# Kernel optimization log

Hardware: AMD Instinct MI355X
Metric: run time of the kernel (lower is better)

Reference implementation:

```python
import jax, jax.numpy as jnp
import numpy as np

N = 8192        # nodes
E = 262144      # edges (avg degree 32)
IN_CH = 256
CH = 128
SLOPE = 0.2     # PyG GATv2Conv default negative_slope


def gatv2(x, src, dst, wl, wr, att, b):
    """Single-head GATv2Conv (PyG defaults: share_weights=False, self-loops
    already appended to src/dst). x: [N, in]; wl, wr: [out, in]; att: [out]."""
    xl = x @ wl.T                      # [N, out] source-side transform (x_j)
    xr = x @ wr.T                      # [N, out] target-side transform (x_i)
    # per-edge attention logit: att . LeakyReLU(x_l[src] + x_r[dst])
    e = jax.nn.leaky_relu(xl[src] + xr[dst], SLOPE) @ att   # [E']
    # segment softmax over incoming edges of each target node
    m = jax.ops.segment_max(e, dst, num_segments=N)
    p = jnp.exp(e - m[dst])
    s = jax.ops.segment_sum(p, dst, num_segments=N)
    alpha = p / s[dst]                 # every node has a self-loop -> s > 0
    out = jax.ops.segment_sum(alpha[:, None] * xl[src], dst, num_segments=N)
    return out + b


def setup_inputs() -> dict:
    key = jax.random.key(0)
    ks = jax.random.split(key, 2 + 5 * 3)
    inp = {
        "x": jax.random.normal(ks[0], (N, IN_CH), dtype=jnp.float32),
        "edge_index": jax.random.randint(ks[1], (2, E), 0, N, dtype=jnp.int64),
    }
    dims = [(CH, IN_CH), (2 * CH, CH), (CH, 2 * CH), (CH, 2 * CH), (IN_CH, CH)]
    ki = 2
    for i, (oc, ic) in enumerate(dims, start=1):
        sc = (2.0 / (ic + oc)) ** 0.5  # glorot-ish
        inp[f"w{i}l"] = jax.random.normal(ks[ki], (oc, ic), dtype=jnp.float32) * sc
        inp[f"w{i}r"] = jax.random.normal(ks[ki + 1], (oc, ic), dtype=jnp.float32) * sc
        inp[f"a{i}"] = jax.random.normal(ks[ki + 2], (oc,), dtype=jnp.float32) * sc
        inp[f"b{i}"] = jnp.zeros((oc,), dtype=jnp.float32)
        ki += 3
    return inp


def reference(x, edge_index,
              w1l, w1r, a1, b1,
              w2l, w2r, a2, b2,
              w3l, w3r, a3, b3,
              w4l, w4r, a4, b4,
              w5l, w5r, a5, b5):
    loops = jnp.arange(N, dtype=edge_index.dtype)
    src = jnp.concatenate([edge_index[0], loops])   # add_self_loops=True
    dst = jnp.concatenate([edge_index[1], loops])
    h = jax.nn.relu(gatv2(x, src, dst, w1l, w1r, a1, b1))          # [N, CH]
    z = jax.nn.relu(gatv2(h, src, dst, w2l, w2r, a2, b2))          # [N, 2CH]
    re = jax.nn.relu(gatv2(z, src, dst, w3l, w3r, a3, b3))         # [N, CH]
    recon_edge = jax.nn.sigmoid(re @ re.T)                         # [N, N]
    xd = jax.nn.relu(gatv2(z, src, dst, w4l, w4r, a4, b4))         # [N, CH]
    x_rec = jax.nn.relu(gatv2(xd, src, dst, w5l, w5r, a5, b5))     # [N, IN_CH]
    return recon_edge, x_rec, z
```

## Files before the change

### kernel.cpp

```cpp
#include <hip/hip_runtime.h>
#include <hip/hip_bf16.h>
#include <math.h>

#define N_NODES 8192
#define N_EDGES 262144
#define EP (N_EDGES + N_NODES)
#define SLOPE 0.2f

typedef short bf16x8 __attribute__((ext_vector_type(8)));
typedef short short4v __attribute__((ext_vector_type(4)));
typedef float f32x4 __attribute__((ext_vector_type(4)));

__global__ void extract_hist(const int* __restrict__ raw,
                             int* __restrict__ esrc, int* __restrict__ edst,
                             int* __restrict__ counts) {
    __shared__ int sflag;
    int t = threadIdx.x;
    if (t < 64) {
        unsigned long long b = __ballot(raw[2 * t + 1] != 0);
        if (t == 0) sflag = (b == 0ULL) ? 1 : 0;
    }
    __syncthreads();
    int i64f = sflag;
    int k = blockIdx.x * blockDim.x + t;
    if (k >= N_EDGES) return;
    int s, d;
    if (i64f) {
        s = raw[2 * (size_t)k];
        d = raw[2 * ((size_t)N_EDGES + k)];
    } else {
        s = raw[k];
        d = raw[N_EDGES + k];
    }
    esrc[k] = s;
    edst[k] = d;
    atomicAdd(&counts[d], 1);
}

__global__ void scan_k(const int* __restrict__ counts, int* __restrict__ row_ptr) {
    __shared__ int part[256];
    int t = threadIdx.x;
    int base = t * 32;
    int loc[32];
    int s = 0;
    for (int i = 0; i < 32; ++i) { loc[i] = s; s += counts[base + i] + 1; }
    part[t] = s;
    __syncthreads();
    for (int off = 1; off < 256; off <<= 1) {
        int tmp = (t >= off) ? part[t - off] : 0;
        __syncthreads();
        part[t] += tmp;
        __syncthreads();
    }
    int incl = part[t];
    int excl = incl - s;
    for (int i = 0; i < 32; ++i) row_ptr[base + i] = excl + loc[i];
    if (t == 255) row_ptr[N_NODES] = incl;
}

__global__ void scatter_k(const int* __restrict__ esrc, const int* __restrict__ edst,
                          const int* __restrict__ row_ptr, int* __restrict__ cursor,
                          int* __restrict__ ssrc) {
    int k = blockIdx.x * blockDim.x + threadIdx.x;
    if (k >= EP) return;
    int s, d;
    if (k < N_EDGES) { s = esrc[k]; d = edst[k]; }
    else             { s = d = k - N_EDGES; }
    int pos = row_ptr[d] + atomicAdd(&cursor[d], 1);
    ssrc[pos] = s;
}

struct WPrep {
    const float* wl[5];
    const float* wr[5];
    int oc[5];
    int lk[5];
};

__global__ void prep_all(WPrep P, const float* __restrict__ x,
                         short* __restrict__ W3all, short* __restrict__ A3) {
    int gid = blockIdx.x * blockDim.x + threadIdx.x;
    if (gid < 524288) {
        int r = gid >> 6;
        int c4 = (gid & 63) << 2;
        f32x4 a = *(const f32x4*)&x[((size_t)r << 8) + c4];
        short4v h4, l4;
#pragma unroll
        for (int j = 0; j < 4; ++j) {
            __hip_bfloat16 hb = __float2bfloat16(a[j]);
            float hf = __bfloat162float(hb);
            __hip_bfloat16 lb = __float2bfloat16(a[j] - hf);
            h4[j] = *(short*)&hb;
            l4[j] = *(short*)&lb;
        }
        size_t ro = (size_t)r * 768;
        *(short4v*)&A3[ro + c4] = h4;
        *(short4v*)&A3[ro + 256 + c4] = l4;
        *(short4v*)&A3[ro + 512 + c4] = h4;
    } else {
        int g = gid - 524288;
        int l = g >> 16;
        if (l >= 5) return;
        int rem = g & 65535;
        int lk = P.lk[l], K = 1 << lk;
        int r = rem >> lk, c = rem & (K - 1);
        int OC = P.oc[l];
        const float* w = (r < OC) ? P.wl[l] : P.wr[l];
        int rr = (r < OC) ? r : r - OC;
        float a = w[((size_t)rr << lk) + c];
        __hip_bfloat16 hb = __float2bfloat16(a);
        float hf = __bfloat162float(hb);
        __hip_bfloat16 lb = __float2bfloat16(a - hf);
        size_t ro = (size_t)l * 196608 + (size_t)r * 3 * K;
        W3all[ro + c] = *(short*)&hb;
        W3all[ro + K + c] = *(short*)&hb;
        W3all[ro + 2 * K + c] = *(short*)&lb;
    }
}

#if __has_builtin(__builtin_amdgcn_global_load_lds)
#define GL16(gsrc, lbase, lofs)                                                       \
    __builtin_amdgcn_global_load_lds((const __attribute__((address_space(1))) void*)(gsrc), \
                                     (__attribute__((address_space(3))) void*)(lbase), 16, 0, 0)
#else
#define GL16(gsrc, lbase, lofs) (*(bf16x8*)((lbase) + (lofs)) = *(const bf16x8*)(gsrc))
#endif

__global__ __launch_bounds__(256) void gemm_bf16_nt(const short* __restrict__ A3,
                                                    const short* __restrict__ W3,
                                                    float* __restrict__ C,
                                                    int K3, int N2) {
    __shared__ __align__(16) short As[2][4096];
    __shared__ __align__(16) short Bs[2][4096];
    int tid = threadIdx.x;
    int gx = gridDim.x;
    int lgx = (gx == 8) ? 3 : 2;
    int orig = blockIdx.x + (blockIdx.y << lgx);
    int nwg = gx << 7;
    int swzb = (orig & 7) * (nwg >> 3) + (orig >> 3);
    int bx = swzb & (gx - 1), by = swzb >> lgx;
    int i0 = by * 64, j0 = bx * 64;

    int wave = tid >> 6, lane = tid & 63;
    int b0 = wave * 1024 + lane * 16;
    int row0 = b0 >> 7;
    int rb0 = b0 & 127;
    int scb = rb0 ^ ((row0 & 7) << 4);
    const short* gA0 = A3 + (size_t)(i0 + row0) * K3 + (scb >> 1);
    const short* gA1 = A3 + (size_t)(i0 + row0 + 32) * K3 + (scb >> 1);
    const short* gB0 = W3 + (size_t)(j0 + row0) * K3 + (scb >> 1);
    const short* gB1 = W3 + (size_t)(j0 + row0 + 32) * K3 + (scb >> 1);
    int lofs = lane * 8;

#define STAGE(pb, k0s)                                      \
    do {                                                    \
        GL16(gA0 + (k0s), &As[pb][wave * 512], lofs);       \
        GL16(gA1 + (k0s), &As[pb][2048 + wave * 512], lofs);\
        GL16(gB0 + (k0s), &Bs[pb][wave * 512], lofs);       \
        GL16(gB1 + (k0s), &Bs[pb][2048 + wave * 512], lofs);\
    } while (0)

    int wr = (wave >> 1) * 32, wc = (wave & 1) * 32;
    int lm = lane & 15, quad = lane >> 4;
    f32x4 acc[2][2] = {};
    int nt = K3 >> 6;
    STAGE(0, 0);
    int cur = 0;
    for (int t = 0; t < nt; ++t) {
        if (t + 1 < nt) {
            STAGE(cur ^ 1, (t + 1) << 6);
            asm volatile("s_waitcnt vmcnt(4)" ::: "memory");
        } else {
            asm volatile("s_waitcnt vmcnt(0)" ::: "memory");
        }
        __builtin_amdgcn_s_barrier();
        __builtin_amdgcn_sched_barrier(0);
        const char* Ab = (const char*)&As[cur][0];
        const char* Bb = (const char*)&Bs[cur][0];
#pragma unroll
        for (int ks = 0; ks < 2; ++ks) {
            int kb = ks * 64 + quad * 16;
            bf16x8 a[2], b[2];
#pragma unroll
            for (int u = 0; u < 2; ++u) {
                int r = wr + u * 16 + lm;
                a[u] = *(const bf16x8*)(Ab + (((r << 7) | kb) ^ ((r & 7) << 4)));
            }
#pragma unroll
            for (int v = 0; v < 2; ++v) {
                int r = wc + v * 16 + lm;
                b[v] = *(const bf16x8*)(Bb + (((r << 7) | kb) ^ ((r & 7) << 4)));
            }
#pragma unroll
            for (int u = 0; u < 2; ++u)
#pragma unroll
                for (int v = 0; v < 2; ++v)
                    acc[u][v] = __builtin_amdgcn_mfma_f32_16x16x32_bf16(a[u], b[v], acc[u][v], 0, 0, 0);
        }
        __builtin_amdgcn_sched_barrier(0);
        __builtin_amdgcn_s_barrier();
        cur ^= 1;
    }
#undef STAGE
#pragma unroll
    for (int u = 0; u < 2; ++u)
#pragma unroll
        for (int v = 0; v < 2; ++v)
#pragma unroll
            for (int r = 0; r < 4; ++r) {
                int row = i0 + wr + u * 16 + quad * 4 + r;
                int col = j0 + wc + v * 16 + lm;
                C[(size_t)row * N2 + col] = acc[u][v][r];
            }
}

#define LSTR 136

__global__ __launch_bounds__(256) void recon_sym(const unsigned short* __restrict__ Rb,
                                                 float* __restrict__ C) {
    __shared__ __align__(16) short Sh[2 * 128 * LSTR];
    short* As = Sh;
    short* Bs = Sh + 128 * LSTR;
    int tid = threadIdx.x;
    int orig = blockIdx.x;
    int s = (orig & 7) * 260 + (orig >> 3);
    float ff = 64.5f - sqrtf(64.5f * 64.5f - 2.0f * (float)s);
    int bi = (int)ff;
    while (bi > 0 && 64 * bi - bi * (bi - 1) / 2 > s) --bi;
    while (64 * (bi + 1) - (bi + 1) * bi / 2 <= s) ++bi;
    int bj = bi + (s - (64 * bi - bi * (bi - 1) / 2));
    int i0 = bi * 128, j0 = bj * 128;
    const short* R = (const short*)Rb;
#pragma unroll
    for (int c = 0; c < 8; ++c) {
        int idx = tid + c * 256;
        int row = idx >> 4, col = (idx & 15) * 8;
        *(bf16x8*)(&As[row * LSTR + col]) = *(const bf16x8*)(&R[(size_t)(i0 + row) * 128 + col]);
        *(bf16x8*)(&Bs[row * LSTR + col]) = *(const bf16x8*)(&R[(size_t)(j0 + row) * 128 + col]);
    }
    __syncthreads();
    int wave = tid >> 6, lane = tid & 63;
    int wr = (wave >> 1) * 64, wc = (wave & 1) * 64;
    int lm = lane & 15, quad = lane >> 4;
    f32x4 acc[4][4] = {};
#pragma unroll
    for (int ks = 0; ks < 4; ++ks) {
        int ko = ks * 32 + quad * 8;
        bf16x8 a[4], b[4];
#pragma unroll
        for (int u = 0; u < 4; ++u)
            a[u] = *(const bf16x8*)(&As[(wr + u * 16 + lm) * LSTR + ko]);
#pragma unroll
        for (int v = 0; v < 4; ++v)
            b[v] = *(const bf16x8*)(&Bs[(wc + v * 16 + lm) * LSTR + ko]);
#pragma unroll
        for (int u = 0; u < 4; ++u)
#pragma unroll
            for (int v = 0; v < 4; ++v)
                acc[u][v] = __builtin_amdgcn_mfma_f32_16x16x32_bf16(a[u], b[v], acc[u][v], 0, 0, 0);
    }
#pragma unroll
    for (int u = 0; u < 4; ++u)
#pragma unroll
        for (int v = 0; v < 4; ++v)
#pragma unroll
            for (int r = 0; r < 4; ++r) {
                acc[u][v][r] = 1.0f / (1.0f + __expf(-acc[u][v][r]));
                int row = i0 + wr + u * 16 + quad * 4 + r;
                int col = j0 + wc + v * 16 + lm;
                C[(size_t)row * 8192 + col] = acc[u][v][r];
            }
    if (bi != bj) {
        __syncthreads();
        float* T = (float*)Sh;
#pragma unroll
        for (int u = 0; u < 4; ++u)
#pragma unroll
            for (int v = 0; v < 4; ++v)
#pragma unroll
                for (int r = 0; r < 4; ++r)
                    T[(wr + u * 16 + quad * 4 + r) * 129 + (wc + v * 16 + lm)] = acc[u][v][r];
        __syncthreads();
#pragma unroll
        for (int it = 0; it < 64; ++it) {
            int idx = tid + it * 256;
            int rp = idx >> 7, cp = idx & 127;
            C[(size_t)(j0 + rp) * 8192 + (i0 + cp)] = T[cp * 129 + rp];
        }
    }
}

struct GatP {
    const float* att; const float* bias;
    float* outf; short* a3; unsigned short* rb;
    int xlo, xro;
};

__global__ __launch_bounds__(256) void gat128(const int* __restrict__ row_ptr,
                                              const int* __restrict__ ssrc,
                                              const float* __restrict__ XLR, int str,
                                              GatP P0, GatP P1) {
    __shared__ float sacc[8][128];
    __shared__ float ss[8];
    int d = blockIdx.x & (N_NODES - 1);
    GatP P = (blockIdx.x >= N_NODES) ? P1 : P0;
    int t = threadIdx.x, ln = t & 31, hw = t >> 5;
    int beg = row_ptr[d], end = row_ptr[d + 1];
    const float* XL = XLR + P.xlo;
    f32x4 at = *(const f32x4*)&P.att[ln * 4];
    f32x4 xr = *(const f32x4*)&XLR[(size_t)d * str + P.xro + ln * 4];
    float s = 0.0f;
    f32x4 acc = {0.0f, 0.0f, 0.0f, 0.0f};
    int p = beg + hw;
    for (; p + 8 < end; p += 16) {
        int s0 = ssrc[p], s1 = ssrc[p + 8];
        f32x4 v0 = *(const f32x4*)&XL[(size_t)s0 * str + ln * 4];
        f32x4 v1 = *(const f32x4*)&XL[(size_t)s1 * str + ln * 4];
        float e0 = 0.0f, e1 = 0.0f;
#pragma unroll
        for (int j = 0; j < 4; ++j) {
            float u0 = v0[j] + xr[j]; u0 = (u0 > 0.0f) ? u0 : SLOPE * u0; e0 += u0 * at[j];
            float u1 = v1[j] + xr[j]; u1 = (u1 > 0.0f) ? u1 : SLOPE * u1; e1 += u1 * at[j];
        }
#pragma unroll
        for (int off = 16; off; off >>= 1) {
            e0 += __shfl_xor(e0, off, 32);
            e1 += __shfl_xor(e1, off, 32);
        }
        float q0 = __expf(e0), q1 = __expf(e1);
        s += q0 + q1;
#pragma unroll
        for (int j = 0; j < 4; ++j) acc[j] += q0 * v0[j] + q1 * v1[j];
    }
    if (p < end) {
        int si = ssrc[p];
        f32x4 v = *(const f32x4*)&XL[(size_t)si * str + ln * 4];
        float e = 0.0f;
#pragma unroll
        for (int j = 0; j < 4; ++j) {
            float u = v[j] + xr[j];
            u = (u > 0.0f) ? u : SLOPE * u;
            e += u * at[j];
        }
#pragma unroll
        for (int off = 16; off; off >>= 1) e += __shfl_xor(e, off, 32);
        float q = __expf(e);
        s += q;
#pragma unroll
        for (int j = 0; j < 4; ++j) acc[j] += q * v[j];
    }
    *(f32x4*)&sacc[hw][ln * 4] = acc;
    if (ln == 0) ss[hw] = s;
    __syncthreads();
    if (t < 128) {
        float tot = 0.0f, st = 0.0f;
#pragma unroll
        for (int w = 0; w < 8; ++w) { tot += sacc[w][t]; st += ss[w]; }
        float val = fmaxf(tot / st + P.bias[t], 0.0f);
        if (P.outf) P.outf[(size_t)d * 128 + t] = val;
        if (P.a3) {
            __hip_bfloat16 hb = __float2bfloat16(val);
            float hf = __bfloat162float(hb);
            __hip_bfloat16 lb = __float2bfloat16(val - hf);
            size_t ro = (size_t)d * 384;
            P.a3[ro + t] = *(short*)&hb;
            P.a3[ro + 128 + t] = *(short*)&lb;
            P.a3[ro + 256 + t] = *(short*)&hb;
        }
        if (P.rb) {
            __hip_bfloat16 hb = __float2bfloat16(val);
            P.rb[d * 128 + t] = *(unsigned short*)&hb;
        }
    }
}

__global__ __launch_bounds__(256) void gat256(const int* __restrict__ row_ptr,
                                              const int* __restrict__ ssrc,
                                              const float* __restrict__ XLR, int str,
                                              const float* __restrict__ att,
                                              const float* __restrict__ bias,
                                              float* __restrict__ outf,
                                              short* __restrict__ a3,
                                              int xlo, int xro) {
    __shared__ float sacc[4][256];
    __shared__ float ss[4];
    int d = blockIdx.x, t = threadIdx.x;
    int lane = t & 63, wave = t >> 6;
    int beg = row_ptr[d], end = row_ptr[d + 1];
    const float* XL = XLR + xlo;
    f32x4 at = *(const f32x4*)&att[lane * 4];
    f32x4 xr = *(const f32x4*)&XLR[(size_t)d * str + xro + lane * 4];
    float s = 0.0f;
    f32x4 acc = {0.0f, 0.0f, 0.0f, 0.0f};
    int p = beg + wave;
    for (; p + 4 < end; p += 8) {
        int s0 = ssrc[p], s1 = ssrc[p + 4];
        f32x4 v0 = *(const f32x4*)&XL[(size_t)s0 * str + lane * 4];
        f32x4 v1 = *(const f32x4*)&XL[(size_t)s1 * str + lane * 4];
        float e0 = 0.0f, e1 = 0.0f;
#pragma unroll
        for (int j = 0; j < 4; ++j) {
            float u0 = v0[j] + xr[j]; u0 = (u0 > 0.0f) ? u0 : SLOPE * u0; e0 += u0 * at[j];
            float u1 = v1[j] + xr[j]; u1 = (u1 > 0.0f) ? u1 : SLOPE * u1; e1 += u1 * at[j];
        }
#pragma unroll
        for (int off = 32; off; off >>= 1) {
            e0 += __shfl_xor(e0, off, 64);
            e1 += __shfl_xor(e1, off, 64);
        }
        float q0 = __expf(e0), q1 = __expf(e1);
        s += q0 + q1;
#pragma unroll
        for (int j = 0; j < 4; ++j) acc[j] += q0 * v0[j] + q1 * v1[j];
    }
    if (p < end) {
        int si = ssrc[p];
        f32x4 v = *(const f32x4*)&XL[(size_t)si * str + lane * 4];
        float e = 0.0f;
#pragma unroll
        for (int j = 0; j < 4; ++j) {
            float u = v[j] + xr[j];
            u = (u > 0.0f) ? u : SLOPE * u;
            e += u * at[j];
        }
#pragma unroll
        for (int off = 32; off; off >>= 1) e += __shfl_xor(e, off, 64);
        float q = __expf(e);
        s += q;
#pragma unroll
        for (int j = 0; j < 4; ++j) acc[j] += q * v[j];
    }
    *(f32x4*)&sacc[wave][lane * 4] = acc;
    if (lane == 0) ss[wave] = s;
    __syncthreads();
    float tot = 0.0f, st = 0.0f;
#pragma unroll
    for (int w = 0; w < 4; ++w) { tot += sacc[w][t]; st += ss[w]; }
    float val = fmaxf(tot / st + bias[t], 0.0f);
    if (outf) outf[(size_t)d * 256 + t] = val;
    if (a3) {
        __hip_bfloat16 hb = __float2bfloat16(val);
        float hf = __bfloat162float(hb);
        __hip_bfloat16 lb = __float2bfloat16(val - hf);
        size_t ro = (size_t)d * 768;
        a3[ro + t] = *(short*)&hb;
        a3[ro + 256 + t] = *(short*)&lb;
        a3[ro + 512 + t] = *(short*)&hb;
    }
}

static inline int ceil_div(int a, int b) { return (a + b - 1) / b; }

extern "C" void kernel_launch(void* const* d_in, const int* in_sizes, int n_in,
                              void* d_out, int out_size, void* d_ws, size_t ws_size,
                              hipStream_t stream) {
    const float* x    = (const float*)d_in[0];
    const int*   eraw = (const int*)d_in[1];

    WPrep P;
    const float* att[5];
    const float* bia[5];
    for (int l = 0; l < 5; ++l) {
        P.wl[l] = (const float*)d_in[2 + 4 * l + 0];
        P.wr[l] = (const float*)d_in[2 + 4 * l + 1];
        att[l]  = (const float*)d_in[2 + 4 * l + 2];
        bia[l]  = (const float*)d_in[2 + 4 * l + 3];
    }
    const int och[5]  = {128, 256, 128, 128, 256};
    const int logK[5] = {8, 7, 8, 8, 7};
    for (int l = 0; l < 5; ++l) { P.oc[l] = och[l]; P.lk[l] = logK[l]; }

    float* outp  = (float*)d_out;
    float* recon = outp;
    float* xrec  = outp + (size_t)67108864;
    float* zout  = outp + (size_t)69206016;

    float* W = (float*)d_ws;
    float* XLR   = W;
    short* A3    = (short*)(W + 4194304);
    short* W3all = (short*)(W + 7340032);
    unsigned short* Rb = (unsigned short*)(W + 7831552);
    int* I       = (int*)(W + 8355840);
    int* counts  = I;
    int* cursor  = I + 8192;
    int* row_ptr = I + 16384;
    int* ssrc    = I + 24577;
    int* esrc    = I + 294913;
    int* edst    = I + 557057;

    hipMemsetAsync(counts, 0, 2 * 8192 * sizeof(int), stream);
    extract_hist<<<ceil_div(N_EDGES, 256), 256, 0, stream>>>(eraw, esrc, edst, counts);
    scan_k<<<1, 256, 0, stream>>>(counts, row_ptr);
    scatter_k<<<ceil_div(EP, 256), 256, 0, stream>>>(esrc, edst, row_ptr, cursor, ssrc);

    prep_all<<<3328, 256, 0, stream>>>(P, x, W3all, A3);

    GatP gp[5];
    for (int l = 0; l < 5; ++l)
        gp[l] = GatP{att[l], bia[l], nullptr, nullptr, nullptr, 0, 0};

    {
        dim3 g(4, 128);
        gemm_bf16_nt<<<g, 256, 0, stream>>>(A3, W3all + 0 * 196608, XLR, 768, 256);
        gp[0].a3 = A3; gp[0].xlo = 0; gp[0].xro = 128;
        gat128<<<N_NODES, 256, 0, stream>>>(row_ptr, ssrc, XLR, 256, gp[0], gp[0]);
    }
    {
        dim3 g(8, 128);
        gemm_bf16_nt<<<g, 256, 0, stream>>>(A3, W3all + 1 * 196608, XLR, 384, 512);
        gat256<<<N_NODES, 256, 0, stream>>>(row_ptr, ssrc, XLR, 512, att[1], bia[1], zout, A3, 0, 256);
    }
    {
        dim3 g(8, 128);
        gemm_bf16_nt<<<g, 256, 0, stream>>>(A3, W3all + 2 * 196608, XLR, 768, 512);
        gp[2].rb = Rb;               gp[2].xlo = 0;   gp[2].xro = 128;
        gp[3].a3 = A3;               gp[3].xlo = 256; gp[3].xro = 384;
        gat128<<<2 * N_NODES, 256, 0, stream>>>(row_ptr, ssrc, XLR, 512, gp[2], gp[3]);
        recon_sym<<<2080, 256, 0, stream>>>(Rb, recon);
    }
    {
        dim3 g(8, 128);
        gemm_bf16_nt<<<g, 256, 0, stream>>>(A3, W3all + 4 * 196608, XLR, 384, 512);
        gat256<<<N_NODES, 256, 0, stream>>>(row_ptr, ssrc, XLR, 512, att[4], bia[4], xrec, nullptr, 0, 256);
    }
}
```

Measured before the change: 534.8 us.

## Store source-side features as bf16 in separate slabs for GAT gathers

The GEMM epilogue now splits its output into a bf16 xl buffer and an fp32 xr buffer, laid out in per-slab contiguous arrays instead of one interleaved fp32 matrix. The GAT aggregation kernels gather bf16 rows (8 elements per lane, with half-warp or 32-lane groups per edge) and convert them to fp32 in registers. This halves the bytes moved by the edge-indexed gathers, which dominate the aggregation cost. The price is reduced precision of xl in both the attention logits and the weighted sum, plus more partial sums to reduce in shared memory.

```diff
diff --git a/kernel.cpp b/kernel.cpp
--- a/kernel.cpp
+++ b/kernel.cpp
@@ -9,6 +9,7 @@
 
 typedef short bf16x8 __attribute__((ext_vector_type(8)));
 typedef short short4v __attribute__((ext_vector_type(4)));
+typedef unsigned short u16x8 __attribute__((ext_vector_type(8)));
 typedef float f32x4 __attribute__((ext_vector_type(4)));
 
 __global__ void extract_hist(const int* __restrict__ raw,
@@ -128,8 +129,9 @@
 
 __global__ __launch_bounds__(256) void gemm_bf16_nt(const short* __restrict__ A3,
                                                     const short* __restrict__ W3,
-                                                    float* __restrict__ C,
-                                                    int K3, int N2) {
+                                                    unsigned short* __restrict__ XLb,
+                                                    float* __restrict__ XRf,
+                                                    int K3, int N2, int ocl, int lgpl) {
     __shared__ __align__(16) short As[2][4096];
     __shared__ __align__(16) short Bs[2][4096];
     int tid = threadIdx.x;
@@ -202,6 +204,7 @@
         cur ^= 1;
     }
 #undef STAGE
+    int plm = (1 << lgpl) - 1;
 #pragma unroll
     for (int u = 0; u < 2; ++u)
 #pragma unroll
@@ -210,7 +213,16 @@
             for (int r = 0; r < 4; ++r) {
                 int row = i0 + wr + u * 16 + quad * 4 + r;
                 int col = j0 + wc + v * 16 + lm;
-                C[(size_t)row * N2 + col] = acc[u][v][r];
+                int slab = col >> lgpl;
+                int wn = col & plm;
+                float val = acc[u][v][r];
+                size_t base = (size_t)slab * N_NODES * ocl + (size_t)row * ocl;
+                if (wn < ocl) {
+                    __hip_bfloat16 hb = __float2bfloat16(val);
+                    XLb[base + wn] = *(unsigned short*)&hb;
+                } else {
+                    XRf[base + wn - ocl] = val;
+                }
             }
 }
 
@@ -293,69 +305,81 @@
 struct GatP {
     const float* att; const float* bias;
     float* outf; short* a3; unsigned short* rb;
-    int xlo, xro;
+    const unsigned short* xlb; const float* xrf;
 };
+
+__device__ __forceinline__ void cvt8(u16x8 w, float* v) {
+#pragma unroll
+    for (int j = 0; j < 8; ++j) v[j] = __uint_as_float(((unsigned)w[j]) << 16);
+}
 
 __global__ __launch_bounds__(256) void gat128(const int* __restrict__ row_ptr,
                                               const int* __restrict__ ssrc,
-                                              const float* __restrict__ XLR, int str,
                                               GatP P0, GatP P1) {
-    __shared__ float sacc[8][128];
-    __shared__ float ss[8];
+    __shared__ float sacc[16][128];
+    __shared__ float ss[16];
     int d = blockIdx.x & (N_NODES - 1);
     GatP P = (blockIdx.x >= N_NODES) ? P1 : P0;
-    int t = threadIdx.x, ln = t & 31, hw = t >> 5;
+    int t = threadIdx.x, ln = t & 15, g = t >> 4;
     int beg = row_ptr[d], end = row_ptr[d + 1];
-    const float* XL = XLR + P.xlo;
-    f32x4 at = *(const f32x4*)&P.att[ln * 4];
-    f32x4 xr = *(const f32x4*)&XLR[(size_t)d * str + P.xro + ln * 4];
-    float s = 0.0f;
-    f32x4 acc = {0.0f, 0.0f, 0.0f, 0.0f};
-    int p = beg + hw;
-    for (; p + 8 < end; p += 16) {
-        int s0 = ssrc[p], s1 = ssrc[p + 8];
-        f32x4 v0 = *(const f32x4*)&XL[(size_t)s0 * str + ln * 4];
-        f32x4 v1 = *(const f32x4*)&XL[(size_t)s1 * str + ln * 4];
+    float xr[8], at[8];
+    {
+        f32x4 a0 = *(const f32x4*)&P.xrf[(size_t)d * 128 + ln * 8];
+        f32x4 a1 = *(const f32x4*)&P.xrf[(size_t)d * 128 + ln * 8 + 4];
+        f32x4 b0 = *(const f32x4*)&P.att[ln * 8];
+        f32x4 b1 = *(const f32x4*)&P.att[ln * 8 + 4];
+#pragma unroll
+        for (int j = 0; j < 4; ++j) { xr[j] = a0[j]; xr[4 + j] = a1[j]; at[j] = b0[j]; at[4 + j] = b1[j]; }
+    }
+    float s = 0.0f, acc[8] = {};
+    int p = beg + g;
+    for (; p + 16 < end; p += 32) {
+        int s0 = ssrc[p], s1 = ssrc[p + 16];
+        float v0[8], v1[8];
+        cvt8(*(const u16x8*)&P.xlb[(size_t)s0 * 128 + ln * 8], v0);
+        cvt8(*(const u16x8*)&P.xlb[(size_t)s1 * 128 + ln * 8], v1);
         float e0 = 0.0f, e1 = 0.0f;
 #pragma unroll
-        for (int j = 0; j < 4; ++j) {
+        for (int j = 0; j < 8; ++j) {
             float u0 = v0[j] + xr[j]; u0 = (u0 > 0.0f) ? u0 : SLOPE * u0; e0 += u0 * at[j];
             float u1 = v1[j] + xr[j]; u1 = (u1 > 0.0f) ? u1 : SLOPE * u1; e1 += u1 * at[j];
         }
 #pragma unroll
-        for (int off = 16; off; off >>= 1) {
-            e0 += __shfl_xor(e0, off, 32);
-            e1 += __shfl_xor(e1, off, 32);
+        for (int off = 8; off; off >>= 1) {
+            e0 += __shfl_xor(e0, off, 64);
+            e1 += __shfl_xor(e1, off, 64);
         }
         float q0 = __expf(e0), q1 = __expf(e1);
         s += q0 + q1;
 #pragma unroll
-        for (int j = 0; j < 4; ++j) acc[j] += q0 * v0[j] + q1 * v1[j];
+        for (int j = 0; j < 8; ++j) acc[j] += q0 * v0[j] + q1 * v1[j];
     }
     if (p < end) {
         int si = ssrc[p];
-        f32x4 v = *(const f32x4*)&XL[(size_t)si * str + ln * 4];
+        float v[8];
+        cvt8(*(const u16x8*)&P.xlb[(size_t)si * 128 + ln * 8], v);
         float e = 0.0f;
 #pragma unroll
-        for (int j = 0; j < 4; ++j) {
+        for (int j = 0; j < 8; ++j) {
             float u = v[j] + xr[j];
             u = (u > 0.0f) ? u : SLOPE * u;
             e += u * at[j];
         }
 #pragma unroll
-        for (int off = 16; off; off >>= 1) e += __shfl_xor(e, off, 32);
+        for (int off = 8; off; off >>= 1) e += __shfl_xor(e, off, 64);
         float q = __expf(e);
         s += q;
 #pragma unroll
-        for (int j = 0; j < 4; ++j) acc[j] += q * v[j];
-    }
-    *(f32x4*)&sacc[hw][ln * 4] = acc;
-    if (ln == 0) ss[hw] = s;
+        for (int j = 0; j < 8; ++j) acc[j] += q * v[j];
+    }
+#pragma unroll
+    for (int j = 0; j < 8; ++j) sacc[g][ln * 8 + j] = acc[j];
+    if (ln == 0) ss[g] = s;
     __syncthreads();
     if (t < 128) {
         float tot = 0.0f, st = 0.0f;
 #pragma unroll
-        for (int w = 0; w < 8; ++w) { tot += sacc[w][t]; st += ss[w]; }
+        for (int w = 0; w < 16; ++w) { tot += sacc[w][t]; st += ss[w]; }
         float val = fmaxf(tot / st + P.bias[t], 0.0f);
         if (P.outf) P.outf[(size_t)d * 128 + t] = val;
         if (P.a3) {
@@ -376,76 +400,86 @@
 
 __global__ __launch_bounds__(256) void gat256(const int* __restrict__ row_ptr,
                                               const int* __restrict__ ssrc,
-                                              const float* __restrict__ XLR, int str,
+                                              const unsigned short* __restrict__ xlb,
+                                              const float* __restrict__ xrf,
                                               const float* __restrict__ att,
                                               const float* __restrict__ bias,
                                               float* __restrict__ outf,
-                                              short* __restrict__ a3,
-                                              int xlo, int xro) {
-    __shared__ float sacc[4][256];
-    __shared__ float ss[4];
+                                              short* __restrict__ a3) {
+    __shared__ float sacc[8][256];
+    __shared__ float ss[8];
     int d = blockIdx.x, t = threadIdx.x;
-    int lane = t & 63, wave = t >> 6;
+    int ln = t & 31, g = t >> 5;
     int beg = row_ptr[d], end = row_ptr[d + 1];
-    const float* XL = XLR + xlo;
-    f32x4 at = *(const f32x4*)&att[lane * 4];
-    f32x4 xr = *(const f32x4*)&XLR[(size_t)d * str + xro + lane * 4];
-    float s = 0.0f;
-    f32x4 acc = {0.0f, 0.0f, 0.0f, 0.0f};
-    int p = beg + wave;
-    for (; p + 4 < end; p += 8) {
-        int s0 = ssrc[p], s1 = ssrc[p + 4];
-        f32x4 v0 = *(const f32x4*)&XL[(size_t)s0 * str + lane * 4];
-        f32x4 v1 = *(const f32x4*)&XL[(size_t)s1 * str + lane * 4];
+    float xr[8], at[8];
+    {
+        f32x4 a0 = *(const f32x4*)&xrf[(size_t)d * 256 + ln * 8];
+        f32x4 a1 = *(const f32x4*)&xrf[(size_t)d * 256 + ln * 8 + 4];
+        f32x4 b0 = *(const f32x4*)&att[ln * 8];
+        f32x4 b1 = *(const f32x4*)&att[ln * 8 + 4];
+#pragma unroll
+        for (int j = 0; j < 4; ++j) { xr[j] = a0[j]; xr[4 + j] = a1[j]; at[j] = b0[j]; at[4 + j] = b1[j]; }
+    }
+    float s = 0.0f, acc[8] = {};
+    int p = beg + g;
+    for (; p + 8 < end; p += 16) {
+        int s0 = ssrc[p], s1 = ssrc[p + 8];
+        float v0[8], v1[8];
+        cvt8(*(const u16x8*)&xlb[(size_t)s0 * 256 + ln * 8], v0);
+        cvt8(*(const u16x8*)&xlb[(size_t)s1 * 256 + ln * 8], v1);
         float e0 = 0.0f, e1 = 0.0f;
 #pragma unroll
-        for (int j = 0; j < 4; ++j) {
+        for (int j = 0; j < 8; ++j) {
             float u0 = v0[j] + xr[j]; u0 = (u0 > 0.0f) ? u0 : SLOPE * u0; e0 += u0 * at[j];
             float u1 = v1[j] + xr[j]; u1 = (u1 > 0.0f) ? u1 : SLOPE * u1; e1 += u1 * at[j];
         }
 #pragma unroll
-        for (int off = 32; off; off >>= 1) {
+        for (int off = 16; off; off >>= 1) {
             e0 += __shfl_xor(e0, off, 64);
             e1 += __shfl_xor(e1, off, 64);
         }
         float q0 = __expf(e0), q1 = __expf(e1);
         s += q0 + q1;
 #pragma unroll
-        for (int j = 0; j < 4; ++j) acc[j] += q0 * v0[j] + q1 * v1[j];
+        for (int j = 0; j < 8; ++j) acc[j] += q0 * v0[j] + q1 * v1[j];
     }
     if (p < end) {
         int si = ssrc[p];
-        f32x4 v = *(const f32x4*)&XL[(size_t)si * str + lane * 4];
+        float v[8];
+        cvt8(*(const u16x8*)&xlb[(size_t)si * 256 + ln * 8], v);
         float e = 0.0f;
 #pragma unroll
-        for (int j = 0; j < 4; ++j) {
+        for (int j = 0; j < 8; ++j) {
             float u = v[j] + xr[j];
             u = (u > 0.0f) ? u : SLOPE * u;
             e += u * at[j];
         }
 #pragma unroll
-        for (int off = 32; off; off >>= 1) e += __shfl_xor(e, off, 64);
+        for (int off = 16; off; off >>= 1) e += __shfl_xor(e, off, 64);
         float q = __expf(e);
         s += q;
 #pragma unroll
-        for (int j = 0; j < 4; ++j) acc[j] += q * v[j];
-    }
-    *(f32x4*)&sacc[wave][lane * 4] = acc;
-    if (lane == 0) ss[wave] = s;
+        for (int j = 0; j < 8; ++j) acc[j] += q * v[j];
+    }
+#pragma unroll
+    for (int j = 0; j < 8; ++j) sacc[g][ln * 8 + j] = acc[j];
+    if (ln == 0) ss[g] = s;
     __syncthreads();
-    float tot = 0.0f, st = 0.0f;
-#pragma unroll
-    for (int w = 0; w < 4; ++w) { tot += sacc[w][t]; st += ss[w]; }
-    float val = fmaxf(tot / st + bias[t], 0.0f);
-    if (outf) outf[(size_t)d * 256 + t] = val;
-    if (a3) {
-        __hip_bfloat16 hb = __float2bfloat16(val);
-        float hf = __bfloat162float(hb);
-        __hip_bfloat16 lb = __float2bfloat16(val - hf);
-        size_t ro = (size_t)d * 768;
-        a3[ro + t] = *(short*)&hb;
-        a3[ro + 256 + t] = *(short*)&lb;
-        a3[ro + 512 + t] = *(short*)&hb;
+    {
+        float tot = 0.0f, st = 0.0f;
+#pragma unroll
+        for (int w = 0; w < 8; ++w) { tot += sacc[w][t]; st += ss[w]; }
+        float val = fmaxf(tot / st + bias[t], 0.0f);
+        if (outf) outf[(size_t)d * 256 + t] = val;
+        if (a3) {
+            __hip_bfloat16 hb = __float2bfloat16(val);
+            float hf = __bfloat162float(hb);
+            __hip_bfloat16 lb = __float2bfloat16(val - hf);
+            size_t ro = (size_t)d * 768;
+            a3[ro + t] = *(short*)&hb;
+            a3[ro + 256 + t] = *(short*)&lb;
+            a3[ro + 512 + t] = *(short*)&hb;
+        }
     }
 }
 
@@ -476,11 +510,12 @@
     float* zout  = outp + (size_t)69206016;
 
     float* W = (float*)d_ws;
-    float* XLR   = W;
-    short* A3    = (short*)(W + 4194304);
-    short* W3all = (short*)(W + 7340032);
-    unsigned short* Rb = (unsigned short*)(W + 7831552);
-    int* I       = (int*)(W + 8355840);
+    unsigned short* XLb = (unsigned short*)W;
+    float* XRf   = W + 1048576;
+    short* A3    = (short*)(W + 3145728);
+    short* W3all = (short*)(W + 6291456);
+    unsigned short* Rb = (unsigned short*)(W + 6782976);
+    int* I       = (int*)(W + 7307264);
     int* counts  = I;
     int* cursor  = I + 8192;
     int* row_ptr = I + 16384;
@@ -495,32 +530,28 @@
 
     prep_all<<<3328, 256, 0, stream>>>(P, x, W3all, A3);
 
-    GatP gp[5];
-    for (int l = 0; l < 5; ++l)
-        gp[l] = GatP{att[l], bia[l], nullptr, nullptr, nullptr, 0, 0};
-
     {
         dim3 g(4, 128);
-        gemm_bf16_nt<<<g, 256, 0, stream>>>(A3, W3all + 0 * 196608, XLR, 768, 256);
-        gp[0].a3 = A3; gp[0].xlo = 0; gp[0].xro = 128;
-        gat128<<<N_NODES, 256, 0, stream>>>(row_ptr, ssrc, XLR, 256, gp[0], gp[0]);
+        gemm_bf16_nt<<<g, 256, 0, stream>>>(A3, W3all + 0 * 196608, XLb, XRf, 768, 256, 128, 8);
+        GatP g0{att[0], bia[0], nullptr, A3, nullptr, XLb, XRf};
+        gat128<<<N_NODES, 256, 0, stream>>>(row_ptr, ssrc, g0, g0);
     }
     {
         dim3 g(8, 128);
-        gemm_bf16_nt<<<g, 256, 0, stream>>>(A3, W3all + 1 * 196608, XLR, 384, 512);
-        gat256<<<N_NODES, 256, 0, stream>>>(row_ptr, ssrc, XLR, 512, att[1], bia[1], zout, A3, 0, 256);
+        gemm_bf16_nt<<<g, 256, 0, stream>>>(A3, W3all + 1 * 196608, XLb, XRf, 384, 512, 256, 9);
+        gat256<<<N_NODES, 256, 0, stream>>>(row_ptr, ssrc, XLb, XRf, att[1], bia[1], zout, A3);
     }
     {
         dim3 g(8, 128);
-        gemm_bf16_nt<<<g, 256, 0, stream>>>(A3, W3all + 2 * 196608, XLR, 768, 512);
-        gp[2].rb = Rb;               gp[2].xlo = 0;   gp[2].xro = 128;
-        gp[3].a3 = A3;               gp[3].xlo = 256; gp[3].xro = 384;
-        gat128<<<2 * N_NODES, 256, 0, stream>>>(row_ptr, ssrc, XLR, 512, gp[2], gp[3]);
+        gemm_bf16_nt<<<g, 256, 0, stream>>>(A3, W3all + 2 * 196608, XLb, XRf, 768, 512, 128, 8);
+        GatP g2{att[2], bia[2], nullptr, nullptr, Rb, XLb, XRf};
+        GatP g3{att[3], bia[3], nullptr, A3, nullptr, XLb + (size_t)N_NODES * 128, XRf + (size_t)N_NODES * 128};
+        gat128<<<2 * N_NODES, 256, 0, stream>>>(row_ptr, ssrc, g2, g3);
         recon_sym<<<2080, 256, 0, stream>>>(Rb, recon);
     }
     {
         dim3 g(8, 128);
-        gemm_bf16_nt<<<g, 256, 0, stream>>>(A3, W3all + 4 * 196608, XLR, 384, 512);
-        gat256<<<N_NODES, 256, 0, stream>>>(row_ptr, ssrc, XLR, 512, att[4], bia[4], xrec, nullptr, 0, 256);
-    }
-}
+        gemm_bf16_nt<<<g, 256, 0, stream>>>(A3, W3all + 4 * 196608, XLb, XRf, 384, 512, 256, 9);
+        gat256<<<N_NODES, 256, 0, stream>>>(row_ptr, ssrc, XLb, XRf, att[4], bia[4], xrec, nullptr);
+    }
+}
```

Result: faster. 521.7 us (-2.5%).
